# Optimization experiments

Measured on AMD Instinct MI355X. Metric: run time of the kernel, lower is better.

The kernel has to match this reference:

```python
import jax, jax.numpy as jnp
import numpy as np

N = 4096       # num nodes
E = 131072     # num edges (avg degree 32)
IN = 128       # in_channels
H = 256        # hidden_channels
NC = 16        # num_classes
NH = 4         # num_heads
HD = H // NH   # head dim
EPS = 1e-5


def setup_inputs() -> dict:
    key = jax.random.key(0)
    ks = jax.random.split(key, 16)
    p = lambda k, sh, s=0.05: jax.random.normal(k, sh, jnp.float32) * s
    return {
        "x": jax.random.normal(ks[0], (N, IN), jnp.float32),
        "edge_index": jax.random.randint(ks[1], (2, E), 0, N),
        "edge_attr": jax.random.uniform(ks[2], (E,), jnp.float32),
        # GCN layers
        "W_gcn1": p(ks[3], (IN, H)), "b_gcn1": jnp.zeros((H,), jnp.float32),
        "W_gcn2": p(ks[4], (H, H)), "b_gcn2": jnp.zeros((H,), jnp.float32),
        # Transformer encoder layer (post-norm, batch_first)
        "in_proj_w": p(ks[5], (3 * H, H)), "in_proj_b": jnp.zeros((3 * H,), jnp.float32),
        "out_proj_w": p(ks[6], (H, H)), "out_proj_b": jnp.zeros((H,), jnp.float32),
        "ln1_g": jnp.ones((H,), jnp.float32), "ln1_b": jnp.zeros((H,), jnp.float32),
        "ffn_w1": p(ks[7], (H, 4 * H)), "ffn_b1": jnp.zeros((4 * H,), jnp.float32),
        "ffn_w2": p(ks[8], (4 * H, H)), "ffn_b2": jnp.zeros((H,), jnp.float32),
        "ln2_g": jnp.ones((H,), jnp.float32), "ln2_b": jnp.zeros((H,), jnp.float32),
        # classifier head
        "W_cls": p(ks[9], (H, NC)), "b_cls": jnp.zeros((NC,), jnp.float32),
        # semantic decoder
        "W_d1": p(ks[10], (H, 2 * H)), "b_d1": jnp.zeros((2 * H,), jnp.float32),
        "W_d2": p(ks[11], (2 * H, 3)), "b_d2": jnp.zeros((3,), jnp.float32),
    }


def gcn_conv(x, edge_index, edge_weight, W, b):
    """PyG GCNConv: add self-loops, symmetric norm, gather-matmul-scatter."""
    n = x.shape[0]
    src, dst = edge_index[0], edge_index[1]
    loop = jnp.arange(n)
    src_f = jnp.concatenate([src, loop])
    dst_f = jnp.concatenate([dst, loop])
    ew_f = jnp.concatenate([edge_weight, jnp.ones((n,), x.dtype)])
    deg = jax.ops.segment_sum(ew_f, dst_f, num_segments=n)
    dinv = jnp.where(deg > 0, jax.lax.rsqrt(deg), 0.0)
    norm = dinv[src_f] * ew_f * dinv[dst_f]            # [E+N]
    h = x @ W                                          # [N,H]
    out = jax.ops.segment_sum(norm[:, None] * h[src_f], dst_f, num_segments=n)
    return out + b


def layer_norm(x, g, b):
    mu = jnp.mean(x, axis=-1, keepdims=True)
    var = jnp.mean(jnp.square(x - mu), axis=-1, keepdims=True)
    return (x - mu) * jax.lax.rsqrt(var + EPS) * g + b


def transformer_layer(x, in_proj_w, in_proj_b, out_proj_w, out_proj_b,
                      ln1_g, ln1_b, ffn_w1, ffn_b1, ffn_w2, ffn_b2, ln2_g, ln2_b):
    # Self-attention (seq = all N nodes, batch of 1), eval mode (no dropout)
    qkv = x @ in_proj_w.T + in_proj_b                  # [N,3H]
    q, k, v = jnp.split(qkv, 3, axis=-1)
    q = q.reshape(-1, NH, HD) * (1.0 / np.sqrt(HD))
    k = k.reshape(-1, NH, HD)
    v = v.reshape(-1, NH, HD)
    scores = jnp.einsum("nhd,mhd->hnm", q, k)          # [NH,N,N]
    attn = jax.nn.softmax(scores, axis=-1)
    ctx = jnp.einsum("hnm,mhd->nhd", attn, v).reshape(-1, H)
    attn_out = ctx @ out_proj_w.T + out_proj_b
    x = layer_norm(x + attn_out, ln1_g, ln1_b)         # post-norm
    ffn = jax.nn.relu(x @ ffn_w1 + ffn_b1) @ ffn_w2 + ffn_b2
    return layer_norm(x + ffn, ln2_g, ln2_b)


def reference(x, edge_index, edge_attr,
              W_gcn1, b_gcn1, W_gcn2, b_gcn2,
              in_proj_w, in_proj_b, out_proj_w, out_proj_b,
              ln1_g, ln1_b, ffn_w1, ffn_b1, ffn_w2, ffn_b2, ln2_g, ln2_b,
              W_cls, b_cls, W_d1, b_d1, W_d2, b_d2):
    x_local = jax.nn.relu(gcn_conv(x, edge_index, edge_attr, W_gcn1, b_gcn1))
    # F.dropout with training=False is identity
    x_local = gcn_conv(x_local, edge_index, edge_attr, W_gcn2, b_gcn2)
    x_global = transformer_layer(x_local, in_proj_w, in_proj_b, out_proj_w,
                                 out_proj_b, ln1_g, ln1_b, ffn_w1, ffn_b1,
                                 ffn_w2, ffn_b2, ln2_g, ln2_b)
    x_final = x_local + x_global
    out_cls = jax.nn.log_softmax(x_final @ W_cls + b_cls, axis=1)
    out_reco = jax.nn.sigmoid(jax.nn.relu(x_final @ W_d1 + b_d1) @ W_d2 + b_d2)
    return (out_cls, out_reco)
```

## Files before the change

### kernel.cpp

```cpp
#include <hip/hip_runtime.h>
#include <hip/hip_bf16.h>

#define N_NODES 4096
#define N_EDGES 131072
#define KSPLIT 8

typedef short bf16x8 __attribute__((ext_vector_type(8)));
typedef float f32x4  __attribute__((ext_vector_type(4)));

#if __has_builtin(__builtin_amdgcn_exp2f)
#define EXP2F __builtin_amdgcn_exp2f
#else
#define EXP2F exp2f
#endif

#define QSCL 0.1803368801111743f

static __device__ __forceinline__ float b2f(__hip_bfloat16 x) { return __bfloat162float(x); }
static __device__ __forceinline__ __hip_bfloat16 f2b(float x) { return __float2bfloat16(x); }
static __device__ __forceinline__ short f2bs(float x) {
    __hip_bfloat16 h = __float2bfloat16(x);
    return *reinterpret_cast<short*>(&h);
}
static __device__ __forceinline__ float us2f(ushort u) {
    union { unsigned i; float f; } x; x.i = ((unsigned)u) << 16; return x.f;
}
static __device__ __forceinline__ unsigned pack2(float lo, float hi) {
    return (unsigned)(ushort)f2bs(lo) | ((unsigned)(ushort)f2bs(hi) << 16);
}

static __device__ __forceinline__ float rmax16(float v) {
    v = fmaxf(v, __shfl_xor(v, 1));
    v = fmaxf(v, __shfl_xor(v, 2));
    v = fmaxf(v, __shfl_xor(v, 4));
    v = fmaxf(v, __shfl_xor(v, 8));
    return v;
}
static __device__ __forceinline__ float rsum16(float v) {
    v += __shfl_xor(v, 1);
    v += __shfl_xor(v, 2);
    v += __shfl_xor(v, 4);
    v += __shfl_xor(v, 8);
    return v;
}
static __device__ __forceinline__ int is_f32(const unsigned* ln1g_raw) {
    return ln1g_raw[0] == 0x3F800000u ? 1 : 0;
}
static __device__ __forceinline__ int is_i64(const unsigned* ei_raw) {
    unsigned acc = 0;
#pragma unroll
    for (int j = 1; j < 32; j += 2) acc |= ei_raw[j];
    return acc == 0u ? 1 : 0;
}

struct Ptrs24 { const void* p[24]; };

#define CAST_TOTAL 1681171

__global__ __launch_bounds__(256) void cast_all(Ptrs24 ptrs, const unsigned* __restrict__ ln1g_raw,
                                                __hip_bfloat16* __restrict__ canon,
                                                float* __restrict__ deg, int* __restrict__ cnt) {
    const int gi = blockIdx.x * 256 + threadIdx.x;
    if (gi < N_NODES) { deg[gi] = 1.0f; cnt[gi] = 0; }
    const int sizes[24] = {524288,131072,32768,256,65536,256,196608,768,65536,256,
                           256,256,262144,1024,262144,256,256,256,4096,16,
                           131072,512,1536,3};
    const long i0 = (long)gi * 8;
    if (i0 >= CAST_TOTAL) return;
    const int f32 = is_f32(ln1g_raw);
    int off = (int)i0, seg = 0, base = 0;
    bool done = false;
#pragma unroll
    for (int s = 0; s < 24; s++) {
        if (!done) {
            if (off < sizes[s]) { seg = s; done = true; }
            else { off -= sizes[s]; base += sizes[s]; }
        }
    }
    const void* p = ptrs.p[seg];
    ushort ov[8];
    int Rlog = -1, C = 0;
    if (seg == 2)       { Rlog = 7;  C = 256; }
    else if (seg == 4)  { Rlog = 8;  C = 256; }
    else if (seg == 12) { Rlog = 8;  C = 1024; }
    else if (seg == 14) { Rlog = 10; C = 256; }
    else if (seg == 20) { Rlog = 8;  C = 512; }
    if (Rlog >= 0) {
        const int c = off >> Rlog;
        const int k0 = off & ((1 << Rlog) - 1);
#pragma unroll
        for (int j = 0; j < 8; j++) {
            const int src = (k0 + j) * C + c;
            float v = f32 ? ((const float*)p)[src] : us2f(((const ushort*)p)[src]);
            ov[j] = (ushort)f2bs(v);
        }
    } else if (off + 8 > sizes[seg]) {
        for (int j = 0; j < 8; j++) {
            if (off + j < sizes[seg]) {
                float v = f32 ? ((const float*)p)[off + j] : us2f(((const ushort*)p)[off + j]);
                canon[base + off + j] = f2b(v);
            }
        }
        return;
    } else if (f32) {
        uint4 a = *(const uint4*)((const float*)p + off);
        uint4 b = *(const uint4*)((const float*)p + off + 4);
        const float* fa = (const float*)&a;
        const float* fb = (const float*)&b;
#pragma unroll
        for (int j = 0; j < 4; j++) { ov[j] = (ushort)f2bs(fa[j]); ov[4 + j] = (ushort)f2bs(fb[j]); }
    } else {
        uint4 a = *(const uint4*)((const ushort*)p + off);
        *(uint4*)ov = a;
    }
    *(uint4*)((ushort*)canon + base + off) = *(uint4*)ov;
}

static __device__ __forceinline__ int ld_idx(const void* ei, int k, int i64) {
    return i64 ? (int)((const long long*)ei)[k] : ((const int*)ei)[k];
}

__global__ __launch_bounds__(256) void deg_scat_k(const void* __restrict__ ei,
                                                  const __hip_bfloat16* __restrict__ ew,
                                                  float* deg, int* cnt) {
    const int i64 = is_i64((const unsigned*)ei);
    int e = blockIdx.x * 256 + threadIdx.x;
    if (e < N_EDGES) {
        int d = ld_idx(ei, N_EDGES + e, i64);
        atomicAdd(&deg[d], b2f(ew[e]));
        atomicAdd(&cnt[d], 1);
    }
}

__global__ __launch_bounds__(256) void scan_k(const float* __restrict__ deg, float* dinv,
                                              int* cnt, int* rowptr) {
    __shared__ int ss[256];
    const int t = threadIdx.x;
    const int base = t * 16;
    int loc[16];
    int run = 0;
#pragma unroll
    for (int j = 0; j < 16; j++) { loc[j] = run; run += cnt[base + j]; }
    ss[t] = run;
    __syncthreads();
    for (int off = 1; off < 256; off <<= 1) {
        int v = (t >= off) ? ss[t - off] : 0;
        __syncthreads();
        ss[t] += v;
        __syncthreads();
    }
    int pre = (t == 0) ? 0 : ss[t - 1];
#pragma unroll
    for (int j = 0; j < 16; j++) rowptr[base + j] = pre + loc[j];
    if (t == 255) rowptr[N_NODES] = pre + run;
    for (int i = t; i < N_NODES; i += 256) {
        float dg = deg[i];
        dinv[i] = dg > 0.f ? rsqrtf(dg) : 0.f;
        cnt[i] = 0;
    }
}

__global__ __launch_bounds__(256) void fill_k(const void* __restrict__ ei,
                                              const __hip_bfloat16* __restrict__ ew,
                                              const float* __restrict__ dinv,
                                              const int* __restrict__ rowptr,
                                              int* cur, int* csrc, float* cw) {
    const int i64 = is_i64((const unsigned*)ei);
    int e = blockIdx.x * 256 + threadIdx.x;
    if (e < N_EDGES) {
        int s = ld_idx(ei, e, i64), d = ld_idx(ei, N_EDGES + e, i64);
        int p = atomicAdd(&cur[d], 1);
        int slot = rowptr[d] + p;
        csrc[slot] = s;
        cw[slot] = dinv[s] * b2f(ew[e]) * dinv[d];
    }
}

template <bool RELU>
__global__ __launch_bounds__(256) void gcn_agg(const __hip_bfloat16* __restrict__ hf,
                                               const float* __restrict__ dinv,
                                               const int* __restrict__ rowptr,
                                               const int* __restrict__ csrc,
                                               const float* __restrict__ cw,
                                               const __hip_bfloat16* __restrict__ bias,
                                               __hip_bfloat16* __restrict__ out) {
    const int t = threadIdx.x;
    const int n = blockIdx.x * 4 + (t >> 6);
    const int c0 = (t & 63) * 4;
    const ushort* hp = (const ushort*)hf;
    const float di = dinv[n];
    float acc[4];
    {
        ushort4 own = *(const ushort4*)(hp + (size_t)n * 256 + c0);
        ushort4 bv  = *(const ushort4*)((const ushort*)bias + c0);
        const float dii = di * di;
        acc[0] = fmaf(dii, us2f(own.x), us2f(bv.x));
        acc[1] = fmaf(dii, us2f(own.y), us2f(bv.y));
        acc[2] = fmaf(dii, us2f(own.z), us2f(bv.z));
        acc[3] = fmaf(dii, us2f(own.w), us2f(bv.w));
    }
    int p = rowptr[n];
    const int end = rowptr[n + 1];
    for (; p + 4 <= end; p += 4) {
        int s0 = csrc[p], s1 = csrc[p + 1], s2 = csrc[p + 2], s3 = csrc[p + 3];
        float w0 = cw[p], w1 = cw[p + 1], w2 = cw[p + 2], w3 = cw[p + 3];
        ushort4 v0 = *(const ushort4*)(hp + (size_t)s0 * 256 + c0);
        ushort4 v1 = *(const ushort4*)(hp + (size_t)s1 * 256 + c0);
        ushort4 v2 = *(const ushort4*)(hp + (size_t)s2 * 256 + c0);
        ushort4 v3 = *(const ushort4*)(hp + (size_t)s3 * 256 + c0);
        acc[0] = fmaf(w0, us2f(v0.x), acc[0]); acc[1] = fmaf(w0, us2f(v0.y), acc[1]);
        acc[2] = fmaf(w0, us2f(v0.z), acc[2]); acc[3] = fmaf(w0, us2f(v0.w), acc[3]);
        acc[0] = fmaf(w1, us2f(v1.x), acc[0]); acc[1] = fmaf(w1, us2f(v1.y), acc[1]);
        acc[2] = fmaf(w1, us2f(v1.z), acc[2]); acc[3] = fmaf(w1, us2f(v1.w), acc[3]);
        acc[0] = fmaf(w2, us2f(v2.x), acc[0]); acc[1] = fmaf(w2, us2f(v2.y), acc[1]);
        acc[2] = fmaf(w2, us2f(v2.z), acc[2]); acc[3] = fmaf(w2, us2f(v2.w), acc[3]);
        acc[0] = fmaf(w3, us2f(v3.x), acc[0]); acc[1] = fmaf(w3, us2f(v3.y), acc[1]);
        acc[2] = fmaf(w3, us2f(v3.z), acc[2]); acc[3] = fmaf(w3, us2f(v3.w), acc[3]);
    }
    for (; p < end; p++) {
        int s = csrc[p];
        float wgt = cw[p];
        ushort4 v = *(const ushort4*)(hp + (size_t)s * 256 + c0);
        acc[0] = fmaf(wgt, us2f(v.x), acc[0]); acc[1] = fmaf(wgt, us2f(v.y), acc[1]);
        acc[2] = fmaf(wgt, us2f(v.z), acc[2]); acc[3] = fmaf(wgt, us2f(v.w), acc[3]);
    }
    if (RELU) {
#pragma unroll
        for (int j = 0; j < 4; j++) acc[j] = fmaxf(acc[j], 0.f);
    }
    ushort4 o;
    o.x = (ushort)f2bs(acc[0]); o.y = (ushort)f2bs(acc[1]);
    o.z = (ushort)f2bs(acc[2]); o.w = (ushort)f2bs(acc[3]);
    *(ushort4*)((ushort*)out + (size_t)n * 256 + c0) = o;
}

template <bool BIAS, bool RELU>
__global__ __launch_bounds__(256) void gemm64(const __hip_bfloat16* __restrict__ A,
                                              const __hip_bfloat16* __restrict__ Bt,
                                              const __hip_bfloat16* __restrict__ bias,
                                              __hip_bfloat16* __restrict__ C,
                                              int K, int Nn) {
    __shared__ __align__(16) short As[64 * 72];
    __shared__ __align__(16) short Bs[64 * 72];
    const int t = threadIdx.x;
    const int m0 = blockIdx.y * 64, n0 = blockIdx.x * 64;
    const int lane = t & 63, w = t >> 6, li = lane & 15, quad = lane >> 4;
    const int sr = t >> 3, sc = (t & 7) * 8;

    f32x4 acc[4];
#pragma unroll
    for (int i = 0; i < 4; i++) acc[i] = (f32x4){0.f, 0.f, 0.f, 0.f};

    uint4 pa[2], pb[2];
#pragma unroll
    for (int i = 0; i < 2; i++) {
        pa[i] = *(const uint4*)((const ushort*)A + (size_t)(m0 + i * 32 + sr) * K + sc);
        pb[i] = *(const uint4*)((const ushort*)Bt + (size_t)(n0 + i * 32 + sr) * K + sc);
    }

    const int NIT = K >> 6;
    for (int kb = 0; kb < NIT; kb++) {
#pragma unroll
        for (int i = 0; i < 2; i++) {
            *(uint4*)&As[(i * 32 + sr) * 72 + sc] = pa[i];
            *(uint4*)&Bs[(i * 32 + sr) * 72 + sc] = pb[i];
        }
        __syncthreads();
        if (kb + 1 < NIT) {
            const int kbase = (kb + 1) * 64;
#pragma unroll
            for (int i = 0; i < 2; i++) {
                pa[i] = *(const uint4*)((const ushort*)A + (size_t)(m0 + i * 32 + sr) * K + kbase + sc);
                pb[i] = *(const uint4*)((const ushort*)Bt + (size_t)(n0 + i * 32 + sr) * K + kbase + sc);
            }
        }
#pragma unroll
        for (int kk = 0; kk < 64; kk += 32) {
            bf16x8 a = *(const bf16x8*)&As[(w * 16 + li) * 72 + kk + quad * 8];
#pragma unroll
            for (int nt = 0; nt < 4; nt++) {
                bf16x8 b = *(const bf16x8*)&Bs[(nt * 16 + li) * 72 + kk + quad * 8];
                acc[nt] = __builtin_amdgcn_mfma_f32_16x16x32_bf16(a, b, acc[nt], 0, 0, 0);
            }
        }
        __syncthreads();
    }
#pragma unroll
    for (int nt = 0; nt < 4; nt++) {
        const int col = n0 + nt * 16 + li;
        const float bv = BIAS ? b2f(bias[col]) : 0.f;
#pragma unroll
        for (int r = 0; r < 4; r++) {
            const int row = m0 + w * 16 + quad * 4 + r;
            float v = acc[nt][r] + bv;
            if (RELU) v = fmaxf(v, 0.f);
            C[(size_t)row * Nn + col] = f2b(v);
        }
    }
}

template <bool BIAS, bool RELU>
__global__ __launch_bounds__(256) void gemm128(const __hip_bfloat16* __restrict__ A,
                                               const __hip_bfloat16* __restrict__ Bt,
                                               const __hip_bfloat16* __restrict__ bias,
                                               __hip_bfloat16* __restrict__ C,
                                               int K, int Nn) {
    __shared__ __align__(16) short As[128 * 72];
    __shared__ __align__(16) short Bs[128 * 72];
    const int t = threadIdx.x;
    const int m0 = blockIdx.y * 128, n0 = blockIdx.x * 128;
    const int lane = t & 63, w = t >> 6, li = lane & 15, quad = lane >> 4;
    const int wr = (w >> 1) * 64, wc = (w & 1) * 64;
    const int sr = t >> 3, sc = (t & 7) * 8;

    f32x4 acc[16];
#pragma unroll
    for (int i = 0; i < 16; i++) acc[i] = (f32x4){0.f, 0.f, 0.f, 0.f};

    uint4 pa[4], pb[4];
#pragma unroll
    for (int i = 0; i < 4; i++) {
        pa[i] = *(const uint4*)((const ushort*)A + (size_t)(m0 + i * 32 + sr) * K + sc);
        pb[i] = *(const uint4*)((const ushort*)Bt + (size_t)(n0 + i * 32 + sr) * K + sc);
    }

    const int NIT = K >> 6;
    for (int kb = 0; kb < NIT; kb++) {
#pragma unroll
        for (int i = 0; i < 4; i++) {
            *(uint4*)&As[(i * 32 + sr) * 72 + sc] = pa[i];
            *(uint4*)&Bs[(i * 32 + sr) * 72 + sc] = pb[i];
        }
        __syncthreads();
        if (kb + 1 < NIT) {
            const int kbase = (kb + 1) * 64;
#pragma unroll
            for (int i = 0; i < 4; i++) {
                pa[i] = *(const uint4*)((const ushort*)A + (size_t)(m0 + i * 32 + sr) * K + kbase + sc);
                pb[i] = *(const uint4*)((const ushort*)Bt + (size_t)(n0 + i * 32 + sr) * K + kbase + sc);
            }
        }
#pragma unroll
        for (int kk = 0; kk < 64; kk += 32) {
            bf16x8 a[4], b[4];
#pragma unroll
            for (int i = 0; i < 4; i++) {
                a[i] = *(const bf16x8*)&As[(wr + i * 16 + li) * 72 + kk + quad * 8];
                b[i] = *(const bf16x8*)&Bs[(wc + i * 16 + li) * 72 + kk + quad * 8];
            }
#pragma unroll
            for (int am = 0; am < 4; am++)
#pragma unroll
                for (int bn = 0; bn < 4; bn++)
                    acc[am * 4 + bn] = __builtin_amdgcn_mfma_f32_16x16x32_bf16(a[am], b[bn], acc[am * 4 + bn], 0, 0, 0);
        }
        __syncthreads();
    }
#pragma unroll
    for (int am = 0; am < 4; am++)
#pragma unroll
        for (int bn = 0; bn < 4; bn++) {
            const int col = n0 + wc + bn * 16 + li;
            const float bv = BIAS ? b2f(bias[col]) : 0.f;
#pragma unroll
            for (int r = 0; r < 4; r++) {
                const int row = m0 + wr + am * 16 + quad * 4 + r;
                float v = acc[am * 4 + bn][r] + bv;
                if (RELU) v = fmaxf(v, 0.f);
                C[(size_t)row * Nn + col] = f2b(v);
            }
        }
}

__global__ __launch_bounds__(256) void attn_part(const __hip_bfloat16* __restrict__ qkv,
                                                 __hip_bfloat16* __restrict__ Opart,
                                                 float* __restrict__ Lpart) {
    __shared__ __align__(16) short Ks[64 * 72];
    __shared__ __align__(16) short Vt[64 * 72];
    const int t = threadIdx.x;
    const int h = blockIdx.y;
    const int q0 = blockIdx.x * 64;
    const int kz = blockIdx.z;
    const int lane = t & 63, w = t >> 6, li = lane & 15, quad = lane >> 4;
    const ushort* qp = (const ushort*)qkv;

    const int kr0 = t >> 3, kd0 = (t & 7) * 8;
    const int jbeg = kz * (N_NODES / KSPLIT);
    const int jend = jbeg + N_NODES / KSPLIT;

    uint4 kreg0 = *(const uint4*)(qp + (size_t)(jbeg + kr0) * 768 + 256 + h * 64 + kd0);
    uint4 kreg1 = *(const uint4*)(qp + (size_t)(jbeg + 32 + kr0) * 768 + 256 + h * 64 + kd0);
    uint4 vreg0 = *(const uint4*)(qp + (size_t)(jbeg + lane) * 768 + 512 + h * 64 + w * 8);
    uint4 vreg1 = *(const uint4*)(qp + (size_t)(jbeg + lane) * 768 + 512 + h * 64 + (4 + w) * 8);

#pragma unroll
    for (int it = 0; it < 2; it++) {
        int idx = it * 256 + t;
        int r = idx >> 3, d = (idx & 7) * 8;
        uint4 v = *(const uint4*)(qp + (size_t)(q0 + r) * 768 + h * 64 + d);
        const ushort* sv = (const ushort*)&v;
        ushort ov[8];
#pragma unroll
        for (int j = 0; j < 8; j++) ov[j] = (ushort)f2bs(us2f(sv[j]) * QSCL);
        *(uint4*)&Ks[r * 72 + d] = *(uint4*)ov;
    }
    __syncthreads();
    bf16x8 qf0 = *(const bf16x8*)&Ks[(w * 16 + li) * 72 + 0  + quad * 8];
    bf16x8 qf1 = *(const bf16x8*)&Ks[(w * 16 + li) * 72 + 32 + quad * 8];
    __syncthreads();

    f32x4 O[4];
#pragma unroll
    for (int i = 0; i < 4; i++) O[i] = (f32x4){0.f, 0.f, 0.f, 0.f};
    float l_run = 0.f;

    const int srcA = 32 * (quad & 1) + li;
    const int srcB = srcA + 16;
    const int hi_t = (quad >> 1) & 1;

    for (int j0 = jbeg; j0 < jend; j0 += 64) {
        *(uint4*)&Ks[kr0 * 72 + kd0] = kreg0;
        *(uint4*)&Ks[(32 + kr0) * 72 + kd0] = kreg1;
        {
            const short* sv = (const short*)&vreg0;
#pragma unroll
            for (int j = 0; j < 8; j++) Vt[(w * 8 + j) * 72 + lane] = sv[j];
            const short* sw = (const short*)&vreg1;
#pragma unroll
            for (int j = 0; j < 8; j++) Vt[((4 + w) * 8 + j) * 72 + lane] = sw[j];
        }
        __syncthreads();
        if (j0 + 64 < jend) {
            kreg0 = *(const uint4*)(qp + (size_t)(j0 + 64 + kr0) * 768 + 256 + h * 64 + kd0);
            kreg1 = *(const uint4*)(qp + (size_t)(j0 + 96 + kr0) * 768 + 256 + h * 64 + kd0);
            vreg0 = *(const uint4*)(qp + (size_t)(j0 + 64 + lane) * 768 + 512 + h * 64 + w * 8);
            vreg1 = *(const uint4*)(qp + (size_t)(j0 + 64 + lane) * 768 + 512 + h * 64 + (4 + w) * 8);
        }

        f32x4 T[4];
#pragma unroll
        for (int i = 0; i < 4; i++) T[i] = (f32x4){0.f, 0.f, 0.f, 0.f};
#pragma unroll
        for (int nt = 0; nt < 4; nt++) {
            bf16x8 kf0 = *(const bf16x8*)&Ks[(nt * 16 + li) * 72 + 0  + quad * 8];
            bf16x8 kf1 = *(const bf16x8*)&Ks[(nt * 16 + li) * 72 + 32 + quad * 8];
            T[nt] = __builtin_amdgcn_mfma_f32_16x16x32_bf16(kf0, qf0, T[nt], 0, 0, 0);
            T[nt] = __builtin_amdgcn_mfma_f32_16x16x32_bf16(kf1, qf1, T[nt], 0, 0, 0);
        }

        float rs = 0.f;
#pragma unroll
        for (int nt = 0; nt < 4; nt++)
#pragma unroll
            for (int r = 0; r < 4; r++) {
                float p = EXP2F(T[nt][r]);
                T[nt][r] = p;
                rs += p;
            }
        rs += __shfl_xor(rs, 16);
        rs += __shfl_xor(rs, 32);
        l_run += rs;

        unsigned pd[4][2];
#pragma unroll
        for (int nt = 0; nt < 4; nt++) {
            pd[nt][0] = pack2(T[nt][0], T[nt][1]);
            pd[nt][1] = pack2(T[nt][2], T[nt][3]);
        }

#pragma unroll
        for (int c = 0; c < 2; c++) {
            const int tl = 2 * c, th = 2 * c + 1;
            unsigned aL0 = (unsigned)__shfl((int)pd[tl][0], srcA);
            unsigned aL1 = (unsigned)__shfl((int)pd[tl][1], srcA);
            unsigned aH0 = (unsigned)__shfl((int)pd[th][0], srcA);
            unsigned aH1 = (unsigned)__shfl((int)pd[th][1], srcA);
            unsigned bL0 = (unsigned)__shfl((int)pd[tl][0], srcB);
            unsigned bL1 = (unsigned)__shfl((int)pd[tl][1], srcB);
            unsigned bH0 = (unsigned)__shfl((int)pd[th][0], srcB);
            unsigned bH1 = (unsigned)__shfl((int)pd[th][1], srcB);
            unsigned af[4];
            af[0] = hi_t ? aH0 : aL0;
            af[1] = hi_t ? aH1 : aL1;
            af[2] = hi_t ? bH0 : bL0;
            af[3] = hi_t ? bH1 : bL1;
            bf16x8 afrag = *(const bf16x8*)af;
#pragma unroll
            for (int nt2 = 0; nt2 < 4; nt2++) {
                bf16x8 vf = *(const bf16x8*)&Vt[(nt2 * 16 + li) * 72 + c * 32 + quad * 8];
                O[nt2] = __builtin_amdgcn_mfma_f32_16x16x32_bf16(afrag, vf, O[nt2], 0, 0, 0);
            }
        }
        __syncthreads();
    }

    const int hb = kz * 4 + h;
    ushort* ob = (ushort*)Opart + ((size_t)hb * 4096 + q0) * 64;
#pragma unroll
    for (int nt = 0; nt < 4; nt++)
#pragma unroll
        for (int r = 0; r < 4; r++)
            ob[(size_t)(w * 16 + quad * 4 + r) * 64 + nt * 16 + li] = (ushort)f2bs(O[nt][r]);
    if (quad == 0)
        Lpart[(size_t)hb * 4096 + q0 + w * 16 + li] = l_run;
}

__global__ __launch_bounds__(256) void attn_comb(const __hip_bfloat16* __restrict__ Opart,
                                                 const float* __restrict__ Lpart,
                                                 __hip_bfloat16* __restrict__ ctx) {
    const int t = threadIdx.x;
    const int h = blockIdx.y;
    const int row = blockIdx.x * 64 + (t >> 2);
    const int d0 = (t & 3) * 16;
    float L = 0.f;
#pragma unroll
    for (int s = 0; s < KSPLIT; s++) L += Lpart[(size_t)(s * 4 + h) * 4096 + row];
    const float inv = 1.f / L;
    float o[16];
#pragma unroll
    for (int j = 0; j < 16; j++) o[j] = 0.f;
#pragma unroll
    for (int s = 0; s < KSPLIT; s++) {
        const ushort* base = (const ushort*)Opart + ((size_t)(s * 4 + h) * 4096 + row) * 64 + d0;
        uint4 v0 = *(const uint4*)base;
        uint4 v1 = *(const uint4*)(base + 8);
        const ushort* sv0 = (const ushort*)&v0;
        const ushort* sv1 = (const ushort*)&v1;
#pragma unroll
        for (int j = 0; j < 8; j++) {
            o[j]     += us2f(sv0[j]);
            o[8 + j] += us2f(sv1[j]);
        }
    }
    ushort pk[16];
#pragma unroll
    for (int j = 0; j < 16; j++) pk[j] = (ushort)f2bs(o[j] * inv);
    ushort* dst = (ushort*)ctx + (size_t)row * 256 + h * 64 + d0;
    *(uint4*)dst = *(uint4*)pk;
    *(uint4*)(dst + 8) = *(uint4*)(pk + 8);
}

template <bool ADDC>
__global__ __launch_bounds__(256) void ln256(const __hip_bfloat16* __restrict__ A,
                                             const __hip_bfloat16* __restrict__ Bv,
                                             const __hip_bfloat16* __restrict__ gw,
                                             const __hip_bfloat16* __restrict__ bw,
                                             const __hip_bfloat16* __restrict__ Cadd,
                                             __hip_bfloat16* __restrict__ out) {
    __shared__ float red[8];
    const int row = blockIdx.x, c = threadIdx.x;
    const size_t o = (size_t)row * 256 + c;
    float x = b2f(A[o]) + b2f(Bv[o]);
    float s = x;
#pragma unroll
    for (int m = 1; m < 64; m <<= 1) s += __shfl_xor(s, m);
    const int wv = c >> 6;
    if ((c & 63) == 0) red[wv] = s;
    __syncthreads();
    float mu = (red[0] + red[1] + red[2] + red[3]) * (1.f / 256.f);
    float d = x - mu;
    float s2 = d * d;
#pragma unroll
    for (int m = 1; m < 64; m <<= 1) s2 += __shfl_xor(s2, m);
    if ((c & 63) == 0) red[4 + wv] = s2;
    __syncthreads();
    float var = (red[4] + red[5] + red[6] + red[7]) * (1.f / 256.f);
    float y = d * rsqrtf(var + 1e-5f) * b2f(gw[c]) + b2f(bw[c]);
    if (ADDC) y += b2f(Cadd[o]);
    out[o] = f2b(y);
}

__global__ __launch_bounds__(256) void cls_reco(const __hip_bfloat16* __restrict__ xf,
                                                const __hip_bfloat16* __restrict__ Wcls,
                                                const __hip_bfloat16* __restrict__ bcls,
                                                const __hip_bfloat16* __restrict__ Wd1t,
                                                const __hip_bfloat16* __restrict__ bd1,
                                                const __hip_bfloat16* __restrict__ Wd2,
                                                const __hip_bfloat16* __restrict__ bd2,
                                                const unsigned* __restrict__ ln1g_raw,
                                                void* __restrict__ out) {
    __shared__ __align__(16) char smem[49408];
    const int t = threadIdx.x;
    if (blockIdx.x < 256) {
        float* Ws = (float*)smem;
        float* bs = (float*)(smem + 16384);
        for (int i = t; i < 4096; i += 256) Ws[i] = b2f(Wcls[i]);
        if (t < 16) bs[t] = b2f(bcls[t]);
        __syncthreads();
        const int c = t & 15, rl = t >> 4;
        const int row = blockIdx.x * 16 + rl;
        const ushort* xr = (const ushort*)xf + (size_t)row * 256;
        float acc = bs[c];
        for (int k0 = 0; k0 < 256; k0 += 8) {
            uint4 v = *(const uint4*)(xr + k0);
            const ushort* sv = (const ushort*)&v;
#pragma unroll
            for (int j = 0; j < 8; j++) acc = fmaf(us2f(sv[j]), Ws[(k0 + j) * 16 + c], acc);
        }
        float mx = rmax16(acc);
        float se = rsum16(__expf(acc - mx));
        float v = acc - mx - __logf(se);
        const size_t oidx = (size_t)row * 16 + c;
        if (is_f32(ln1g_raw)) ((float*)out)[oidx] = v;
        else                  ((__hip_bfloat16*)out)[oidx] = f2b(v);
    } else {
        short* As = (short*)smem;
        short* Bs = (short*)(smem + 1280);
        float* W2s = (float*)(smem + 42240);
        float (*red)[16][3] = (float (*)[16][3])(smem + 48384);
        const int m0 = (blockIdx.x - 256) * 16;
        const int lane = t & 63, w = t >> 6, li = lane & 15, quad = lane >> 4;
        const ushort* Ap = (const ushort*)xf;
        const ushort* Bp = (const ushort*)Wd1t;
        const int K = 256;

        for (int i = t; i < 1536; i += 256) W2s[i] = b2f(Wd2[i]);

        f32x4 acc[8];
#pragma unroll
        for (int i = 0; i < 8; i++) acc[i] = (f32x4){0.f, 0.f, 0.f, 0.f};

        const int bn = t >> 2, bk0 = (t & 3) * 8;
        const int ar = t >> 2, ak0 = (t & 3) * 8;

        uint4 breg[8];
        uint4 areg;
#pragma unroll
        for (int it2 = 0; it2 < 8; it2++)
            breg[it2] = *(const uint4*)(Bp + (size_t)(it2 * 64 + bn) * K + bk0);
        if (t < 64) areg = *(const uint4*)(Ap + (size_t)(m0 + ar) * K + ak0);

        for (int kb = 0; kb < 8; kb++) {
#pragma unroll
            for (int it2 = 0; it2 < 8; it2++)
                *(uint4*)&Bs[(it2 * 64 + bn) * 40 + bk0] = breg[it2];
            if (t < 64) *(uint4*)&As[ar * 40 + ak0] = areg;
            __syncthreads();
            if (kb + 1 < 8) {
                const int kbase = (kb + 1) * 32;
#pragma unroll
                for (int it2 = 0; it2 < 8; it2++)
                    breg[it2] = *(const uint4*)(Bp + (size_t)(it2 * 64 + bn) * K + kbase + bk0);
                if (t < 64) areg = *(const uint4*)(Ap + (size_t)(m0 + ar) * K + kbase + ak0);
            }
            bf16x8 a = *(const bf16x8*)&As[li * 40 + quad * 8];
#pragma unroll
            for (int nt = 0; nt < 8; nt++) {
                bf16x8 b = *(const bf16x8*)&Bs[(w * 128 + nt * 16 + li) * 40 + quad * 8];
                acc[nt] = __builtin_amdgcn_mfma_f32_16x16x32_bf16(a, b, acc[nt], 0, 0, 0);
            }
            __syncthreads();
        }

        float p3[3][4];
#pragma unroll
        for (int c = 0; c < 3; c++)
#pragma unroll
            for (int r = 0; r < 4; r++) p3[c][r] = 0.f;
#pragma unroll
        for (int nt = 0; nt < 8; nt++) {
            const int col = w * 128 + nt * 16 + li;
            const float bv = b2f(bd1[col]);
            const float w0 = W2s[col * 3 + 0], w1 = W2s[col * 3 + 1], w2 = W2s[col * 3 + 2];
#pragma unroll
            for (int r = 0; r < 4; r++) {
                float hv = fmaxf(acc[nt][r] + bv, 0.f);
                p3[0][r] = fmaf(hv, w0, p3[0][r]);
                p3[1][r] = fmaf(hv, w1, p3[1][r]);
                p3[2][r] = fmaf(hv, w2, p3[2][r]);
            }
        }
#pragma unroll
        for (int c = 0; c < 3; c++)
#pragma unroll
            for (int r = 0; r < 4; r++) {
                float s = rsum16(p3[c][r]);
                if (li == 0) red[w][quad * 4 + r][c] = s;
            }
        __syncthreads();
        if (t < 48) {
            const int rl = t / 3, c = t % 3;
            float s = red[0][rl][c] + red[1][rl][c] + red[2][rl][c] + red[3][rl][c] + b2f(bd2[c]);
            float v = 1.f / (1.f + __expf(-s));
            const size_t oidx = (size_t)(N_NODES * 16) + (size_t)(m0 + rl) * 3 + c;
            if (is_f32(ln1g_raw)) ((float*)out)[oidx] = v;
            else                  ((__hip_bfloat16*)out)[oidx] = f2b(v);
        }
    }
}

extern "C" void kernel_launch(void* const* d_in, const int* in_sizes, int n_in,
                              void* d_out, int out_size, void* d_ws, size_t ws_size,
                              hipStream_t stream) {
    char* ws = (char*)d_ws;
    __hip_bfloat16* canon = (__hip_bfloat16*)(ws + 256);
    float* deg    = (float*)(ws + 3362816);
    int*   cnt    = (int*)  (ws + 3379200);
    int*   rowptr = (int*)  (ws + 3395584);
    float* dinv   = (float*)(ws + 3412224);
    int*   csrc   = (int*)  (ws + 3428608);
    float* cw     = (float*)(ws + 3952896);
    __hip_bfloat16* h     = (__hip_bfloat16*)(ws + 4477184);
    __hip_bfloat16* x1    = (__hip_bfloat16*)(ws + 6574336);
    __hip_bfloat16* xloc  = (__hip_bfloat16*)(ws + 8671488);
    __hip_bfloat16* big   = (__hip_bfloat16*)(ws + 10768640);
    __hip_bfloat16* ctxp  = (__hip_bfloat16*)(ws + 19157248);
    __hip_bfloat16* attno = (__hip_bfloat16*)(ws + 21254400);
    __hip_bfloat16* y1    = (__hip_bfloat16*)(ws + 23351552);
    __hip_bfloat16* xfin  = (__hip_bfloat16*)(ws + 25448704);
    __hip_bfloat16* Opart = (__hip_bfloat16*)(ws + 27545856);
    float* Lpart = (float*)(ws + 6574336);

    const __hip_bfloat16* xc    = canon + 0;
    const __hip_bfloat16* eac   = canon + 524288;
    const __hip_bfloat16* Wg1   = canon + 655360;
    const __hip_bfloat16* bg1   = canon + 688128;
    const __hip_bfloat16* Wg2   = canon + 688384;
    const __hip_bfloat16* bg2   = canon + 753920;
    const __hip_bfloat16* ipw   = canon + 754176;
    const __hip_bfloat16* ipb   = canon + 950784;
    const __hip_bfloat16* opw   = canon + 951552;
    const __hip_bfloat16* opb   = canon + 1017088;
    const __hip_bfloat16* ln1g  = canon + 1017344;
    const __hip_bfloat16* ln1b  = canon + 1017600;
    const __hip_bfloat16* fw1   = canon + 1017856;
    const __hip_bfloat16* fb1   = canon + 1280000;
    const __hip_bfloat16* fw2   = canon + 1281024;
    const __hip_bfloat16* fb2   = canon + 1543168;
    const __hip_bfloat16* ln2g  = canon + 1543424;
    const __hip_bfloat16* ln2b  = canon + 1543680;
    const __hip_bfloat16* Wcls  = canon + 1543936;
    const __hip_bfloat16* bcls  = canon + 1548032;
    const __hip_bfloat16* Wd1   = canon + 1548048;
    const __hip_bfloat16* bd1   = canon + 1679120;
    const __hip_bfloat16* Wd2   = canon + 1679632;
    const __hip_bfloat16* bd2   = canon + 1681168;

    const void* ei = d_in[1];
    const unsigned* ln1g_raw = (const unsigned*)d_in[11];

    Ptrs24 pt;
    {
        const int map[24] = {0,2,3,4,5,6,7,8,9,10,11,12,13,14,15,16,17,18,19,20,21,22,23,24};
        for (int i = 0; i < 24; i++) pt.p[i] = d_in[map[i]];
    }

    const dim3 b256(256);

    cast_all<<<(CAST_TOTAL / 8 + 256) / 256, b256, 0, stream>>>(pt, ln1g_raw, canon, deg, cnt);

    deg_scat_k<<<512, b256, 0, stream>>>(ei, eac, deg, cnt);
    scan_k<<<1, b256, 0, stream>>>(deg, dinv, cnt, rowptr);
    fill_k<<<512, b256, 0, stream>>>(ei, eac, dinv, rowptr, cnt, csrc, cw);

    gemm64<false, false><<<dim3(4, 64), b256, 0, stream>>>(xc, Wg1, nullptr, h, 128, 256);
    gcn_agg<true><<<1024, b256, 0, stream>>>(h, dinv, rowptr, csrc, cw, bg1, x1);
    gemm64<false, false><<<dim3(4, 64), b256, 0, stream>>>(x1, Wg2, nullptr, h, 256, 256);
    gcn_agg<false><<<1024, b256, 0, stream>>>(h, dinv, rowptr, csrc, cw, bg2, xloc);

    gemm128<true, false><<<dim3(6, 32), b256, 0, stream>>>(xloc, ipw, ipb, big, 256, 768);
    attn_part<<<dim3(64, 4, KSPLIT), b256, 0, stream>>>(big, Opart, Lpart);
    attn_comb<<<dim3(64, 4), b256, 0, stream>>>(Opart, Lpart, ctxp);
    gemm64<true, false><<<dim3(4, 64), b256, 0, stream>>>(ctxp, opw, opb, attno, 256, 256);
    ln256<false><<<4096, b256, 0, stream>>>(xloc, attno, ln1g, ln1b, nullptr, y1);
    gemm128<true, true><<<dim3(8, 32), b256, 0, stream>>>(y1, fw1, fb1, big, 256, 1024);
    gemm64<true, false><<<dim3(4, 64), b256, 0, stream>>>(big, fw2, fb2, ctxp, 1024, 256);
    ln256<true><<<4096, b256, 0, stream>>>(y1, ctxp, ln2g, ln2b, xloc, xfin);

    cls_reco<<<512, b256, 0, stream>>>(xfin, Wcls, bcls, Wd1, bd1, Wd2, bd2, ln1g_raw, d_out);
}
```

Baseline: 330.4 us.

## Fuse attention combine into out-proj GEMM, drop gemm128 and register prefetch

Folds the split-K attention combine (sum of partial outputs scaled by the reciprocal of the summed partial normalisers) into the A-tile load of the output-projection GEMM. This removes one launch and the round trip of the ctx buffer through memory, at the cost of each of the four column blocks recomputing the same combine. It also replaces the 128x128 GEMM with the 64x64 GEMM for the QKV and FFN1 projections, and drops the register-prefetch double buffering in gemm64 and attn_part in favour of a plain load, store, sync loop. These last changes simplify the kernels but lose the overlap of global loads with compute and give the large GEMMs less data reuse per tile.

```diff
diff --git a/kernel.cpp b/kernel.cpp
--- a/kernel.cpp
+++ b/kernel.cpp
@@ -245,35 +245,22 @@
     const int t = threadIdx.x;
     const int m0 = blockIdx.y * 64, n0 = blockIdx.x * 64;
     const int lane = t & 63, w = t >> 6, li = lane & 15, quad = lane >> 4;
-    const int sr = t >> 3, sc = (t & 7) * 8;
 
     f32x4 acc[4];
 #pragma unroll
     for (int i = 0; i < 4; i++) acc[i] = (f32x4){0.f, 0.f, 0.f, 0.f};
 
-    uint4 pa[2], pb[2];
-#pragma unroll
-    for (int i = 0; i < 2; i++) {
-        pa[i] = *(const uint4*)((const ushort*)A + (size_t)(m0 + i * 32 + sr) * K + sc);
-        pb[i] = *(const uint4*)((const ushort*)Bt + (size_t)(n0 + i * 32 + sr) * K + sc);
-    }
-
-    const int NIT = K >> 6;
-    for (int kb = 0; kb < NIT; kb++) {
+    for (int k0 = 0; k0 < K; k0 += 64) {
 #pragma unroll
         for (int i = 0; i < 2; i++) {
-            *(uint4*)&As[(i * 32 + sr) * 72 + sc] = pa[i];
-            *(uint4*)&Bs[(i * 32 + sr) * 72 + sc] = pb[i];
-        }
-        __syncthreads();
-        if (kb + 1 < NIT) {
-            const int kbase = (kb + 1) * 64;
-#pragma unroll
-            for (int i = 0; i < 2; i++) {
-                pa[i] = *(const uint4*)((const ushort*)A + (size_t)(m0 + i * 32 + sr) * K + kbase + sc);
-                pb[i] = *(const uint4*)((const ushort*)Bt + (size_t)(n0 + i * 32 + sr) * K + kbase + sc);
-            }
-        }
+            int idx = i * 256 + t;
+            int r = idx >> 3, c8 = (idx & 7) * 8;
+            uint4 va = *(const uint4*)((const ushort*)A + (size_t)(m0 + r) * K + k0 + c8);
+            *(uint4*)&As[r * 72 + c8] = va;
+            uint4 vb = *(const uint4*)((const ushort*)Bt + (size_t)(n0 + r) * K + k0 + c8);
+            *(uint4*)&Bs[r * 72 + c8] = vb;
+        }
+        __syncthreads();
 #pragma unroll
         for (int kk = 0; kk < 64; kk += 32) {
             bf16x8 a = *(const bf16x8*)&As[(w * 16 + li) * 72 + kk + quad * 8];
@@ -297,79 +284,6 @@
             C[(size_t)row * Nn + col] = f2b(v);
         }
     }
-}
-
-template <bool BIAS, bool RELU>
-__global__ __launch_bounds__(256) void gemm128(const __hip_bfloat16* __restrict__ A,
-                                               const __hip_bfloat16* __restrict__ Bt,
-                                               const __hip_bfloat16* __restrict__ bias,
-                                               __hip_bfloat16* __restrict__ C,
-                                               int K, int Nn) {
-    __shared__ __align__(16) short As[128 * 72];
-    __shared__ __align__(16) short Bs[128 * 72];
-    const int t = threadIdx.x;
-    const int m0 = blockIdx.y * 128, n0 = blockIdx.x * 128;
-    const int lane = t & 63, w = t >> 6, li = lane & 15, quad = lane >> 4;
-    const int wr = (w >> 1) * 64, wc = (w & 1) * 64;
-    const int sr = t >> 3, sc = (t & 7) * 8;
-
-    f32x4 acc[16];
-#pragma unroll
-    for (int i = 0; i < 16; i++) acc[i] = (f32x4){0.f, 0.f, 0.f, 0.f};
-
-    uint4 pa[4], pb[4];
-#pragma unroll
-    for (int i = 0; i < 4; i++) {
-        pa[i] = *(const uint4*)((const ushort*)A + (size_t)(m0 + i * 32 + sr) * K + sc);
-        pb[i] = *(const uint4*)((const ushort*)Bt + (size_t)(n0 + i * 32 + sr) * K + sc);
-    }
-
-    const int NIT = K >> 6;
-    for (int kb = 0; kb < NIT; kb++) {
-#pragma unroll
-        for (int i = 0; i < 4; i++) {
-            *(uint4*)&As[(i * 32 + sr) * 72 + sc] = pa[i];
-            *(uint4*)&Bs[(i * 32 + sr) * 72 + sc] = pb[i];
-        }
-        __syncthreads();
-        if (kb + 1 < NIT) {
-            const int kbase = (kb + 1) * 64;
-#pragma unroll
-            for (int i = 0; i < 4; i++) {
-                pa[i] = *(const uint4*)((const ushort*)A + (size_t)(m0 + i * 32 + sr) * K + kbase + sc);
-                pb[i] = *(const uint4*)((const ushort*)Bt + (size_t)(n0 + i * 32 + sr) * K + kbase + sc);
-            }
-        }
-#pragma unroll
-        for (int kk = 0; kk < 64; kk += 32) {
-            bf16x8 a[4], b[4];
-#pragma unroll
-            for (int i = 0; i < 4; i++) {
-                a[i] = *(const bf16x8*)&As[(wr + i * 16 + li) * 72 + kk + quad * 8];
-                b[i] = *(const bf16x8*)&Bs[(wc + i * 16 + li) * 72 + kk + quad * 8];
-            }
-#pragma unroll
-            for (int am = 0; am < 4; am++)
-#pragma unroll
-                for (int bn = 0; bn < 4; bn++)
-                    acc[am * 4 + bn] = __builtin_amdgcn_mfma_f32_16x16x32_bf16(a[am], b[bn], acc[am * 4 + bn], 0, 0, 0);
-        }
-        __syncthreads();
-    }
-#pragma unroll
-    for (int am = 0; am < 4; am++)
-#pragma unroll
-        for (int bn = 0; bn < 4; bn++) {
-            const int col = n0 + wc + bn * 16 + li;
-            const float bv = BIAS ? b2f(bias[col]) : 0.f;
-#pragma unroll
-            for (int r = 0; r < 4; r++) {
-                const int row = m0 + wr + am * 16 + quad * 4 + r;
-                float v = acc[am * 4 + bn][r] + bv;
-                if (RELU) v = fmaxf(v, 0.f);
-                C[(size_t)row * Nn + col] = f2b(v);
-            }
-        }
 }
 
 __global__ __launch_bounds__(256) void attn_part(const __hip_bfloat16* __restrict__ qkv,
@@ -382,22 +296,12 @@
     const int q0 = blockIdx.x * 64;
     const int kz = blockIdx.z;
     const int lane = t & 63, w = t >> 6, li = lane & 15, quad = lane >> 4;
-    const ushort* qp = (const ushort*)qkv;
-
-    const int kr0 = t >> 3, kd0 = (t & 7) * 8;
-    const int jbeg = kz * (N_NODES / KSPLIT);
-    const int jend = jbeg + N_NODES / KSPLIT;
-
-    uint4 kreg0 = *(const uint4*)(qp + (size_t)(jbeg + kr0) * 768 + 256 + h * 64 + kd0);
-    uint4 kreg1 = *(const uint4*)(qp + (size_t)(jbeg + 32 + kr0) * 768 + 256 + h * 64 + kd0);
-    uint4 vreg0 = *(const uint4*)(qp + (size_t)(jbeg + lane) * 768 + 512 + h * 64 + w * 8);
-    uint4 vreg1 = *(const uint4*)(qp + (size_t)(jbeg + lane) * 768 + 512 + h * 64 + (4 + w) * 8);
 
 #pragma unroll
     for (int it = 0; it < 2; it++) {
         int idx = it * 256 + t;
         int r = idx >> 3, d = (idx & 7) * 8;
-        uint4 v = *(const uint4*)(qp + (size_t)(q0 + r) * 768 + h * 64 + d);
+        uint4 v = *(const uint4*)((const ushort*)qkv + (size_t)(q0 + r) * 768 + h * 64 + d);
         const ushort* sv = (const ushort*)&v;
         ushort ov[8];
 #pragma unroll
@@ -418,24 +322,24 @@
     const int srcB = srcA + 16;
     const int hi_t = (quad >> 1) & 1;
 
-    for (int j0 = jbeg; j0 < jend; j0 += 64) {
-        *(uint4*)&Ks[kr0 * 72 + kd0] = kreg0;
-        *(uint4*)&Ks[(32 + kr0) * 72 + kd0] = kreg1;
-        {
-            const short* sv = (const short*)&vreg0;
-#pragma unroll
-            for (int j = 0; j < 8; j++) Vt[(w * 8 + j) * 72 + lane] = sv[j];
-            const short* sw = (const short*)&vreg1;
-#pragma unroll
-            for (int j = 0; j < 8; j++) Vt[((4 + w) * 8 + j) * 72 + lane] = sw[j];
-        }
-        __syncthreads();
-        if (j0 + 64 < jend) {
-            kreg0 = *(const uint4*)(qp + (size_t)(j0 + 64 + kr0) * 768 + 256 + h * 64 + kd0);
-            kreg1 = *(const uint4*)(qp + (size_t)(j0 + 96 + kr0) * 768 + 256 + h * 64 + kd0);
-            vreg0 = *(const uint4*)(qp + (size_t)(j0 + 64 + lane) * 768 + 512 + h * 64 + w * 8);
-            vreg1 = *(const uint4*)(qp + (size_t)(j0 + 64 + lane) * 768 + 512 + h * 64 + (4 + w) * 8);
-        }
+    const int jbeg = kz * (N_NODES / KSPLIT);
+    for (int j0 = jbeg; j0 < jbeg + N_NODES / KSPLIT; j0 += 64) {
+#pragma unroll
+        for (int it = 0; it < 2; it++) {
+            int idx = it * 256 + t;
+            int r = idx >> 3, d = (idx & 7) * 8;
+            uint4 kv = *(const uint4*)((const ushort*)qkv + (size_t)(j0 + r) * 768 + 256 + h * 64 + d);
+            *(uint4*)&Ks[r * 72 + d] = kv;
+        }
+#pragma unroll
+        for (int it = 0; it < 2; it++) {
+            int dblk = it * 4 + w;
+            uint4 vv = *(const uint4*)((const ushort*)qkv + (size_t)(j0 + lane) * 768 + 512 + h * 64 + dblk * 8);
+            const short* sv = (const short*)&vv;
+#pragma unroll
+            for (int j = 0; j < 8; j++) Vt[(dblk * 8 + j) * 72 + lane] = sv[j];
+        }
+        __syncthreads();
 
         f32x4 T[4];
 #pragma unroll
@@ -505,39 +409,78 @@
         Lpart[(size_t)hb * 4096 + q0 + w * 16 + li] = l_run;
 }
 
-__global__ __launch_bounds__(256) void attn_comb(const __hip_bfloat16* __restrict__ Opart,
-                                                 const float* __restrict__ Lpart,
-                                                 __hip_bfloat16* __restrict__ ctx) {
+__global__ __launch_bounds__(256) void opcomb(const __hip_bfloat16* __restrict__ Opart,
+                                              const float* __restrict__ Lpart,
+                                              const __hip_bfloat16* __restrict__ Bt,
+                                              const __hip_bfloat16* __restrict__ bias,
+                                              __hip_bfloat16* __restrict__ C) {
+    __shared__ __align__(16) short As[64 * 72];
+    __shared__ __align__(16) short Bs[64 * 72];
     const int t = threadIdx.x;
-    const int h = blockIdx.y;
-    const int row = blockIdx.x * 64 + (t >> 2);
-    const int d0 = (t & 3) * 16;
-    float L = 0.f;
-#pragma unroll
-    for (int s = 0; s < KSPLIT; s++) L += Lpart[(size_t)(s * 4 + h) * 4096 + row];
-    const float inv = 1.f / L;
-    float o[16];
-#pragma unroll
-    for (int j = 0; j < 16; j++) o[j] = 0.f;
-#pragma unroll
-    for (int s = 0; s < KSPLIT; s++) {
-        const ushort* base = (const ushort*)Opart + ((size_t)(s * 4 + h) * 4096 + row) * 64 + d0;
-        uint4 v0 = *(const uint4*)base;
-        uint4 v1 = *(const uint4*)(base + 8);
-        const ushort* sv0 = (const ushort*)&v0;
-        const ushort* sv1 = (const ushort*)&v1;
-#pragma unroll
-        for (int j = 0; j < 8; j++) {
-            o[j]     += us2f(sv0[j]);
-            o[8 + j] += us2f(sv1[j]);
-        }
-    }
-    ushort pk[16];
-#pragma unroll
-    for (int j = 0; j < 16; j++) pk[j] = (ushort)f2bs(o[j] * inv);
-    ushort* dst = (ushort*)ctx + (size_t)row * 256 + h * 64 + d0;
-    *(uint4*)dst = *(uint4*)pk;
-    *(uint4*)(dst + 8) = *(uint4*)(pk + 8);
+    const int m0 = blockIdx.y * 64, n0 = blockIdx.x * 64;
+    const int lane = t & 63, w = t >> 6, li = lane & 15, quad = lane >> 4;
+    const ushort* Op = (const ushort*)Opart;
+
+    f32x4 acc[4];
+#pragma unroll
+    for (int i = 0; i < 4; i++) acc[i] = (f32x4){0.f, 0.f, 0.f, 0.f};
+
+    const int sr = t >> 3, sc = (t & 7) * 8;
+    const int ar = t >> 2, ac0 = (t & 3) * 16;
+
+    for (int kb = 0; kb < 4; kb++) {
+#pragma unroll
+        for (int i = 0; i < 2; i++) {
+            uint4 vb = *(const uint4*)((const ushort*)Bt + (size_t)(n0 + i * 32 + sr) * 256 + kb * 64 + sc);
+            *(uint4*)&Bs[(i * 32 + sr) * 72 + sc] = vb;
+        }
+        {
+            const int gr = m0 + ar;
+            float L = 0.f;
+#pragma unroll
+            for (int s = 0; s < KSPLIT; s++) L += Lpart[(size_t)(s * 4 + kb) * 4096 + gr];
+            const float inv = 1.f / L;
+            float sum[16];
+#pragma unroll
+            for (int j = 0; j < 16; j++) sum[j] = 0.f;
+#pragma unroll
+            for (int s = 0; s < KSPLIT; s++) {
+                const ushort* ob = Op + ((size_t)(s * 4 + kb) * 4096 + gr) * 64 + ac0;
+                uint4 v0 = *(const uint4*)ob;
+                uint4 v1 = *(const uint4*)(ob + 8);
+                const ushort* s0 = (const ushort*)&v0;
+                const ushort* s1 = (const ushort*)&v1;
+#pragma unroll
+                for (int j = 0; j < 8; j++) { sum[j] += us2f(s0[j]); sum[8 + j] += us2f(s1[j]); }
+            }
+            ushort ov[16];
+#pragma unroll
+            for (int j = 0; j < 16; j++) ov[j] = (ushort)f2bs(sum[j] * inv);
+            *(uint4*)&As[ar * 72 + ac0] = *(uint4*)ov;
+            *(uint4*)&As[ar * 72 + ac0 + 8] = *(uint4*)(ov + 8);
+        }
+        __syncthreads();
+#pragma unroll
+        for (int kk = 0; kk < 64; kk += 32) {
+            bf16x8 a = *(const bf16x8*)&As[(w * 16 + li) * 72 + kk + quad * 8];
+#pragma unroll
+            for (int nt = 0; nt < 4; nt++) {
+                bf16x8 b = *(const bf16x8*)&Bs[(nt * 16 + li) * 72 + kk + quad * 8];
+                acc[nt] = __builtin_amdgcn_mfma_f32_16x16x32_bf16(a, b, acc[nt], 0, 0, 0);
+            }
+        }
+        __syncthreads();
+    }
+#pragma unroll
+    for (int nt = 0; nt < 4; nt++) {
+        const int col = n0 + nt * 16 + li;
+        const float bv = b2f(bias[col]);
+#pragma unroll
+        for (int r = 0; r < 4; r++) {
+            const int row = m0 + w * 16 + quad * 4 + r;
+            C[(size_t)row * 256 + col] = f2b(acc[nt][r] + bv);
+        }
+    }
 }
 
 template <bool ADDC>
@@ -758,12 +701,11 @@
     gemm64<false, false><<<dim3(4, 64), b256, 0, stream>>>(x1, Wg2, nullptr, h, 256, 256);
     gcn_agg<false><<<1024, b256, 0, stream>>>(h, dinv, rowptr, csrc, cw, bg2, xloc);
 
-    gemm128<true, false><<<dim3(6, 32), b256, 0, stream>>>(xloc, ipw, ipb, big, 256, 768);
+    gemm64<true, false><<<dim3(12, 64), b256, 0, stream>>>(xloc, ipw, ipb, big, 256, 768);
     attn_part<<<dim3(64, 4, KSPLIT), b256, 0, stream>>>(big, Opart, Lpart);
-    attn_comb<<<dim3(64, 4), b256, 0, stream>>>(Opart, Lpart, ctxp);
-    gemm64<true, false><<<dim3(4, 64), b256, 0, stream>>>(ctxp, opw, opb, attno, 256, 256);
+    opcomb<<<dim3(4, 64), b256, 0, stream>>>(Opart, Lpart, opw, opb, attno);
     ln256<false><<<4096, b256, 0, stream>>>(xloc, attno, ln1g, ln1b, nullptr, y1);
-    gemm128<true, true><<<dim3(8, 32), b256, 0, stream>>>(y1, fw1, fb1, big, 256, 1024);
+    gemm64<true, true><<<dim3(16, 64), b256, 0, stream>>>(y1, fw1, fb1, big, 256, 1024);
     gemm64<true, false><<<dim3(4, 64), b256, 0, stream>>>(big, fw2, fb2, ctxp, 1024, 256);
     ln256<true><<<4096, b256, 0, stream>>>(y1, ctxp, ln2g, ln2b, xloc, xfin);
 
```

Result: no change. 334.6 us (+1.3%).
